# Optimization experiments

Hardware: AMD Instinct MI355X
Metric: run time of the kernel (lower is better)

The kernel has to match this reference:

```python
import jax, jax.numpy as jnp
import numpy as np


def _ln(z, g, b):
    m = z.mean(-1, keepdims=True)
    v = ((z - m) ** 2).mean(-1, keepdims=True)
    return (z - m) * jax.lax.rsqrt(v + 1e-5) * g + b


def _pe(T, D):
    # standard sinusoidal positional encoding (T, D)
    pos = np.arange(T)[:, None]
    i = np.arange(D // 2)[None, :]
    ang = pos / np.power(10000.0, 2.0 * i / D)
    pe = np.zeros((T, D), dtype=np.float32)
    pe[:, 0::2] = np.sin(ang)
    pe[:, 1::2] = np.cos(ang)
    return jnp.asarray(pe)


def _whconv(z, Hinc, filt, W, b):
    # Wavelet hypergraph convolution: psi diag(filt) psi^{-1} Z W + b
    # psi = heat-kernel wavelet of normalized hypergraph Laplacian, 2nd-order Taylor (K=2, s=1)
    S = Hinc.shape[0]
    Dv = Hinc.sum(1) + 1e-6          # node degrees
    De = Hinc.sum(0) + 1e-6          # hyperedge degrees
    Hn = Hinc * (Dv ** -0.5)[:, None]
    A = (Hn / De[None, :]) @ Hn.T    # Dv^-1/2 H De^-1 H^T Dv^-1/2
    I = jnp.eye(S, dtype=z.dtype)
    L = I - A
    L2 = 0.5 * (L @ L)
    psi = I - L + L2                  # exp(-L) approx
    psi_inv = I + L + L2              # exp(+L) approx
    return psi @ (filt[:, None] * (psi_inv @ z)) @ W + b


def setup_inputs():
    S, T, F, D, NS, E, K = 2048, 64, 16, 256, 4, 128, 32
    key = jax.random.key(0)
    ks = iter(jax.random.split(key, 64))
    nrm = lambda shp: jax.random.normal(next(ks), shp, jnp.float32) * 0.02
    return dict(
        x=jax.random.normal(next(ks), (S, T, F), jnp.float32),
        snapshot=(jax.random.uniform(next(ks), (NS, S, E)) < 0.05).astype(jnp.float32),
        params_snapshot=jax.random.uniform(next(ks), (NS,), jnp.float32, 0.0, 0.99),
        beta=jnp.array([0.33, 0.33, 0.33], jnp.float32),
        W_emb=nrm((F, D)), b_emb=jnp.zeros((D,), jnp.float32),
        Wq=nrm((D, D)), bq=jnp.zeros((D,), jnp.float32),
        Wk=nrm((D, D)), bk=jnp.zeros((D,), jnp.float32),
        Wv=nrm((D, D)), bv=jnp.zeros((D,), jnp.float32),
        Wo=nrm((D, D)), bo=jnp.zeros((D,), jnp.float32),
        ln1_g=jnp.ones((D,), jnp.float32), ln1_b=jnp.zeros((D,), jnp.float32),
        W_int=nrm((D, D)), b_int=jnp.zeros((D,), jnp.float32),
        W_mix=nrm((2 * D, D)), b_mix=jnp.zeros((D,), jnp.float32),
        ln2_g=jnp.ones((D,), jnp.float32), ln2_b=jnp.zeros((D,), jnp.float32),
        Wt=nrm((D, D)), bt=jnp.zeros((D,), jnp.float32), vt=nrm((D,)),
        Wh1=nrm((D, D)), bh1=jnp.zeros((D,), jnp.float32), filt1=jnp.ones((S,), jnp.float32),
        Wh2=nrm((D, D)), bh2=jnp.zeros((D,), jnp.float32), filt2=jnp.ones((S,), jnp.float32),
        Wa=nrm((D, D)), Wb=nrm((D, D)), Wg=nrm((D, D)), bg=jnp.zeros((D,), jnp.float32),
        Wm1=nrm((D, D)), bm1=jnp.zeros((D,), jnp.float32),
        Wm2=nrm((D, 1)), bm2=jnp.zeros((1,), jnp.float32),
        num_edges=K,
    )


def reference(x, snapshot, params_snapshot, beta, W_emb, b_emb, Wq, bq, Wk, bk, Wv, bv,
              Wo, bo, ln1_g, ln1_b, W_int, b_int, W_mix, b_mix, ln2_g, ln2_b,
              Wt, bt, vt, Wh1, bh1, filt1, Wh2, bh2, filt2, Wa, Wb, Wg, bg,
              Wm1, bm1, Wm2, bm2, num_edges):
    S, T, _ = x.shape
    D = W_emb.shape[1]
    H = 8
    dh = D // H
    # feature embedding + positional encoding
    h = x @ W_emb + b_emb + _pe(T, D)
    # intra-stock (per-stock temporal) multi-head self-attention + residual + LN
    q = (h @ Wq + bq).reshape(S, T, H, dh)
    k = (h @ Wk + bk).reshape(S, T, H, dh)
    v = (h @ Wv + bv).reshape(S, T, H, dh)
    att = jax.nn.softmax(jnp.einsum('sqhd,skhd->shqk', q, k) / jnp.sqrt(jnp.float32(dh)), axis=-1)
    o = jnp.einsum('shqk,skhd->sqhd', att, v).reshape(S, T, D) @ Wo + bo
    h = _ln(h + o, ln1_g, ln1_b)
    # intensity function + mixing layer (Linear -> ReLU -> LayerNorm)
    intensity = jax.nn.softplus(h @ W_int + b_int)
    z = jax.nn.relu(jnp.concatenate([h, intensity], axis=-1) @ W_mix + b_mix)
    h = _ln(z, ln2_g, ln2_b)
    # temporal attention pooling: (S,T,D) -> (S,D)
    u = jnp.tanh(h @ Wt + bt)
    a = jax.nn.softmax(u @ vt, axis=-1)          # (S,T)
    xs = jnp.einsum('st,std->sd', a, h)           # (S,D)
    # per-snapshot two-layer wavelet hypergraph conv (dropout = eval identity)
    def per_snap(Hinc):
        r1 = jax.nn.leaky_relu(_whconv(xs, Hinc, filt1, Wh1, bh1), 0.1)
        return _whconv(r1, Hinc, filt2, Wh2, bh2)
    reps = jax.vmap(per_snap)(snapshot)           # (NS,S,D)
    hyper = jnp.einsum('n,nsd->sd', params_snapshot, reps)
    # dynamic graph learning: top-k learned similarity graph
    sim = (xs @ Wa) @ (xs @ Wb).T / jnp.sqrt(jnp.float32(D))
    kth = jax.lax.top_k(sim, num_edges)[0][:, -1]
    Adyn = jax.nn.softmax(jnp.where(sim >= kth[:, None], sim, -jnp.inf), axis=-1)
    dyn = jax.nn.relu(Adyn @ xs @ Wg + bg)
    # fusion ('sum' mode) + MLP head
    w = jax.nn.softmax(beta)
    fused = w[0] * xs + w[1] * dyn + w[2] * hyper
    return jax.nn.relu(fused @ Wm1 + bm1) @ Wm2 + bm2   # (S,1)
```

## Files before the change

kernel.cpp:

```cpp
#include <hip/hip_runtime.h>
#include <math.h>

#define S_ 2048
#define T_ 64
#define F_ 16
#define D_ 256
#define NS_ 4
#define E_ 128
#define H_ 8
#define SD_ (S_*D_)
#define PS 264

#define PK_ATT 0
#define PK_WO  393216
#define PK_WI  524288
#define PK_WT  655360
#define PK_WM  786432
#define PKBASE 11674112

typedef __attribute__((ext_vector_type(8))) short bf16x8;
typedef __attribute__((ext_vector_type(4))) float f32x4;

__device__ __forceinline__ float warp_sum64(float v){
  #pragma unroll
  for (int o=32;o>=1;o>>=1) v += __shfl_xor(v,o);
  return v;
}
__device__ __forceinline__ float warp_max64(float v){
  #pragma unroll
  for (int o=32;o>=1;o>>=1) v = fmaxf(v,__shfl_xor(v,o));
  return v;
}
__device__ __forceinline__ float softplus_f(float v){
  return fmaxf(v,0.f) + log1pf(__expf(-fabsf(v)));
}
__device__ __forceinline__ float tanh_f(float v){
  float t = __expf(-2.f*fabsf(v));
  float r = (1.f-t)/(1.f+t);
  return copysignf(r, v);
}
__device__ __forceinline__ void splitf(float f, short& h, short& l){
  unsigned u = __float_as_uint(f);
  unsigned hb = (u + 0x7FFFu + ((u>>16)&1u)) >> 16;
  float fl = f - __uint_as_float(hb<<16);
  unsigned v = __float_as_uint(fl);
  unsigned lb = (v + 0x7FFFu + ((v>>16)&1u)) >> 16;
  h = (short)hb; l = (short)lb;
}
__device__ __forceinline__ f32x4 mfma3(bf16x8 ah, bf16x8 al, bf16x8 bh, bf16x8 bl, f32x4 c){
  c = __builtin_amdgcn_mfma_f32_16x16x32_bf16(al, bh, c, 0,0,0);
  c = __builtin_amdgcn_mfma_f32_16x16x32_bf16(ah, bl, c, 0,0,0);
  c = __builtin_amdgcn_mfma_f32_16x16x32_bf16(ah, bh, c, 0,0,0);
  return c;
}
__device__ __forceinline__ void afrag_f32(const float* base, int stride, int rbase, int ks, int lane, bf16x8& hi, bf16x8& lo){
  const float* p = base + (rbase + (lane&15))*stride + ks + ((lane>>4)<<3);
  #pragma unroll
  for (int jj=0;jj<8;++jj){ short h,l; splitf(p[jj],h,l); hi[jj]=h; lo[jj]=l; }
}
__device__ __forceinline__ bf16x8 afrag_pk(const short* plane, int rbase, int ks, int lane){
  return *(const bf16x8*)(plane + (rbase + (lane&15))*PS + ks + ((lane>>4)<<3));
}
__device__ __forceinline__ void bfrag_pk(const unsigned* pk, int tile, int lane, bf16x8& hi, bf16x8& lo){
  const unsigned* p = pk + (((tile<<6) + lane)<<3);
  #pragma unroll
  for (int jj=0;jj<8;++jj){ unsigned u=p[jj]; hi[jj]=(short)(u & 0xffffu); lo[jj]=(short)(u>>16); }
}
__device__ __forceinline__ void store_h(short* Hh, short* Hl, int r, int c, float f){
  short h,l; splitf(f,h,l);
  Hh[r*PS+c]=h; Hl[r*PS+c]=l;
}
__device__ __forceinline__ float load_h(const short* Hh, const short* Hl, int r, int c){
  int idx=r*PS+c;
  return __uint_as_float(((unsigned)(unsigned short)Hh[idx])<<16)
       + __uint_as_float(((unsigned)(unsigned short)Hl[idx])<<16);
}

__global__ void pack_all(const float* __restrict__ Wq, const float* __restrict__ Wk,
                         const float* __restrict__ Wv, const float* __restrict__ Wo,
                         const float* __restrict__ Wint, const float* __restrict__ Wt,
                         const float* __restrict__ Wmix, short* __restrict__ pkc){
  int y = blockIdx.y;
  int i = blockIdx.x*256 + threadIdx.x;
  if (y < 3){
    const float* W = (y==0)?Wq:((y==1)?Wk:Wv);
    int jj=i&7, n=(i>>3)&15, q=(i>>7)&3, ntg=(i>>9)&15, kt=i>>13;
    float f = W[(kt*32 + q*8 + jj)*256 + (ntg*16+n)];
    short h,l; splitf(f,h,l);
    int hp = ntg>>2, ntl = ntg&3;
    int base = ((hp*8+kt)*6 + y*2)*2048;
    int local = ntl*512 + (q*16+n)*8 + jj;
    short* dst = pkc + PK_ATT;
    dst[base+local] = h;
    dst[base+2048+local] = l;
  } else {
    const float* W; short* dst; int ib = i;
    if (y==3){W=Wo;   dst=pkc+PK_WO;}
    else if (y==4){W=Wint; dst=pkc+PK_WI;}
    else if (y==5){W=Wt;   dst=pkc+PK_WT;}
    else if (y==6){W=Wmix; dst=pkc+PK_WM;}
    else          {W=Wmix; dst=pkc+PK_WM; ib = i + 65536;}
    int jj=ib&7, n=(ib>>3)&15, q=(ib>>7)&3, ntg=(ib>>9)&15, kt=ib>>13;
    float f = W[(kt*32 + q*8 + jj)*256 + (ntg*16+n)];
    short h,l; splitf(f,h,l);
    int dl = kt*16384 + ntg*512 + (q*16+n)*8 + jj;
    dst[dl] = h; dst[dl+8192] = l;
  }
}

__global__ void pe_kernel(float* __restrict__ pe){
  int i = blockIdx.x*256 + threadIdx.x;
  int t = i >> 8, d = i & 255;
  int ii = d >> 1;
  float w = __expf(-(float)ii * (logf(10000.f)/128.f));
  float ang = (float)t * w;
  pe[i] = (d & 1) ? cosf(ang) : sinf(ang);
}

__launch_bounds__(512,1)
__global__ void stageA_kernel(
    const float* __restrict__ x, const float* __restrict__ pe,
    const float* __restrict__ Wemb, const float* __restrict__ bemb,
    const float* __restrict__ bq, const float* __restrict__ bk, const float* __restrict__ bv,
    const float* __restrict__ bo,
    const float* __restrict__ ln1g, const float* __restrict__ ln1b,
    const float* __restrict__ bint,
    const float* __restrict__ bmix,
    const float* __restrict__ ln2g, const float* __restrict__ ln2b,
    const float* __restrict__ bt,
    const float* __restrict__ vt,
    const short* __restrict__ pkc,
    float* __restrict__ xs)
{
  __shared__ __attribute__((aligned(16))) short hbh[64*PS];
  __shared__ __attribute__((aligned(16))) short hbl[64*PS];
  __shared__ __attribute__((aligned(16))) char smem[85504];

  short*    wst   = (short*)smem;
  unsigned* k2f2  = (unsigned*)smem;
  unsigned* v2f2  = (unsigned*)(smem + 16384);
  float*    qb2   = (float*)(smem + 32768);
  float*    scb2  = (float*)(smem + 50176);
  float*    poolb = (float*)smem;

  const int j  = threadIdx.x;
  const int s  = blockIdx.x;
  const int w  = j >> 6;
  const int lane = j & 63;
  const int m_ = lane & 15, qd = lane >> 4;
  const int rg2 = w >> 1, par = w & 1;
  const int rbase = rg2*16;
  const int rv = w*8;
  const int c0 = lane;

  {
    float* xb = (float*)smem;
    const float* xp = x + (long)s*T_*F_;
    for (int i=j; i<T_*F_; i+=512) xb[i] = xp[i];
  }
  __syncthreads();

  {
    const float* xb = (const float*)smem;
    float acc[8][4];
    #pragma unroll
    for (int r=0;r<8;++r){acc[r][0]=0;acc[r][1]=0;acc[r][2]=0;acc[r][3]=0;}
    #pragma unroll
    for (int k=0;k<F_;++k){
      float w0=Wemb[k*D_+c0], w1=Wemb[k*D_+c0+64], w2=Wemb[k*D_+c0+128], w3=Wemb[k*D_+c0+192];
      #pragma unroll
      for (int r=0;r<8;++r){
        float hv = xb[(rv+r)*F_+k];
        acc[r][0]+=hv*w0; acc[r][1]+=hv*w1; acc[r][2]+=hv*w2; acc[r][3]+=hv*w3;
      }
    }
    float b0=bemb[c0],b1=bemb[c0+64],b2=bemb[c0+128],b3=bemb[c0+192];
    __syncthreads();
    #pragma unroll
    for (int r=0;r<8;++r){
      int t = rv+r;
      store_h(hbh,hbl,t,c0,     acc[r][0]+b0+pe[t*D_+c0]);
      store_h(hbh,hbl,t,c0+64,  acc[r][1]+b1+pe[t*D_+c0+64]);
      store_h(hbh,hbl,t,c0+128, acc[r][2]+b2+pe[t*D_+c0+128]);
      store_h(hbh,hbl,t,c0+192, acc[r][3]+b3+pe[t*D_+c0+192]);
    }
  }
  __syncthreads();

  bf16x8 AH[8], AL[8];
  #pragma unroll
  for (int kt=0;kt<8;++kt){
    AH[kt] = afrag_pk(hbh, rbase, kt*32, lane);
    AL[kt] = afrag_pk(hbl, rbase, kt*32, lane);
  }

  const float rs = 0.17677669529663687f;
  f32x4 co[8];
  #pragma unroll
  for (int t=0;t<8;++t) co[t] = (f32x4){0.f,0.f,0.f,0.f};

  for (int hp=0; hp<4; ++hp){
    f32x4 qa[2],ka[2],va[2];
    #pragma unroll
    for (int t=0;t<2;++t){
      qa[t]=(f32x4){0.f,0.f,0.f,0.f};
      ka[t]=(f32x4){0.f,0.f,0.f,0.f};
      va[t]=(f32x4){0.f,0.f,0.f,0.f};
    }
    bf16x8 pre[3];
    {
      const short* b0 = pkc + PK_ATT + (hp*8)*12288;
      #pragma unroll
      for (int r=0;r<3;++r) pre[r] = *(const bf16x8*)(b0 + (j+r*512)*8);
    }
    for (int kt=0; kt<8; ++kt){
      __syncthreads();
      #pragma unroll
      for (int r=0;r<3;++r) *(bf16x8*)(wst + (j+r*512)*8) = pre[r];
      __syncthreads();
      if (kt<7){
        const short* nb = pkc + PK_ATT + (hp*8+kt+1)*12288;
        #pragma unroll
        for (int r=0;r<3;++r) pre[r] = *(const bf16x8*)(nb + (j+r*512)*8);
      }
      bf16x8 ah = AH[kt], al = AL[kt];
      #pragma unroll
      for (int t=0;t<2;++t){
        int ntl = par*2+t;
        bf16x8 bh,bl;
        bh = *(bf16x8*)(wst +         ntl*512 + lane*8);
        bl = *(bf16x8*)(wst + 2048  + ntl*512 + lane*8);
        qa[t]=mfma3(ah,al,bh,bl,qa[t]);
        bh = *(bf16x8*)(wst + 4096  + ntl*512 + lane*8);
        bl = *(bf16x8*)(wst + 6144  + ntl*512 + lane*8);
        ka[t]=mfma3(ah,al,bh,bl,ka[t]);
        bh = *(bf16x8*)(wst + 8192  + ntl*512 + lane*8);
        bl = *(bf16x8*)(wst + 10240 + ntl*512 + lane*8);
        va[t]=mfma3(ah,al,bh,bl,va[t]);
      }
    }
    __syncthreads();
    #pragma unroll
    for (int t=0;t<2;++t){
      int ntg = par*2+t;
      #pragma unroll
      for (int r=0;r<4;++r){
        int trow = rbase + qd*4 + r;
        int pcp = ntg*16 + m_;
        int head = pcp >> 5;
        int cp = pcp & 31;
        int col = hp*64 + pcp;
        qb2[trow*68 + pcp] = (qa[t][r] + bq[col]) * rs;
        short hS,lS;
        float kv2 = ka[t][r] + bk[col];
        splitf(kv2,hS,lS);
        k2f2[head*2048 + (((trow>>4)*4 + (cp>>3))*16 + (trow&15))*8 + (cp&7)]
            = (unsigned)(unsigned short)hS | ((unsigned)(unsigned short)lS<<16);
        float vv2 = va[t][r] + bv[col];
        splitf(vv2,hS,lS);
        v2f2[head*2048 + ((((trow>>5)*2 + (cp>>4))*4 + ((trow>>3)&3))*16 + (cp&15))*8 + (trow&7)]
            = (unsigned)(unsigned short)hS | ((unsigned)(unsigned short)lS<<16);
      }
    }
    __syncthreads();
    float* scb = scb2 + par*4352;
    {
      bf16x8 ah,al;
      afrag_f32(qb2, 68, rbase, par*32, lane, ah, al);
      f32x4 sc4[4];
      #pragma unroll
      for (int nt=0;nt<4;++nt){
        bf16x8 bh,bl; bfrag_pk(k2f2 + par*2048, nt, lane, bh, bl);
        sc4[nt] = mfma3(ah,al,bh,bl,(f32x4){0.f,0.f,0.f,0.f});
      }
      #pragma unroll
      for (int r=0;r<4;++r){
        float mx = fmaxf(fmaxf(sc4[0][r],sc4[1][r]),fmaxf(sc4[2][r],sc4[3][r]));
        #pragma unroll
        for (int o=8;o>=1;o>>=1) mx = fmaxf(mx, __shfl_xor(mx,o));
        float es = 0.f;
        #pragma unroll
        for (int nt=0;nt<4;++nt){ float e=__expf(sc4[nt][r]-mx); sc4[nt][r]=e; es+=e; }
        #pragma unroll
        for (int o=8;o>=1;o>>=1) es += __shfl_xor(es,o);
        float inv = 1.f/es;
        int trow = rbase + qd*4 + r;
        #pragma unroll
        for (int nt=0;nt<4;++nt) scb[trow*68 + nt*16 + m_] = sc4[nt][r]*inv;
      }
    }
    {
      f32x4 oa[2];
      oa[0]=(f32x4){0.f,0.f,0.f,0.f}; oa[1]=(f32x4){0.f,0.f,0.f,0.f};
      #pragma unroll
      for (int kt=0;kt<2;++kt){
        bf16x8 ah2,al2; afrag_f32(scb, 68, rbase, kt*32, lane, ah2, al2);
        #pragma unroll
        for (int nt=0;nt<2;++nt){
          bf16x8 bh,bl; bfrag_pk(v2f2 + par*2048, kt*2+nt, lane, bh, bl);
          oa[nt]=mfma3(ah2,al2,bh,bl,oa[nt]);
        }
      }
      #pragma unroll
      for (int nt=0;nt<2;++nt){
        #pragma unroll
        for (int r=0;r<4;++r)
          qb2[(rbase+qd*4+r)*68 + par*32 + nt*16 + m_] = oa[nt][r];
      }
    }
    __syncthreads();
    for (int ks=0; ks<2; ++ks){
      bf16x8 ah,al; afrag_f32(qb2, 68, rbase, ks*32, lane, ah, al);
      const short* wob = pkc + PK_WO + (hp*2+ks)*16384 + lane*8;
      #pragma unroll
      for (int t=0;t<8;++t){
        int ntg = 2*t+par;
        bf16x8 bh = *(const bf16x8*)(wob + ntg*512);
        bf16x8 bl = *(const bf16x8*)(wob + 8192 + ntg*512);
        co[t]=mfma3(ah,al,bh,bl,co[t]);
      }
    }
  }

  #pragma unroll
  for (int t=0;t<8;++t){
    int cc = (2*t+par)*16+m_;
    float bov = bo[cc];
    #pragma unroll
    for (int r=0;r<4;++r){
      int row = rbase+qd*4+r;
      store_h(hbh,hbl,row,cc, load_h(hbh,hbl,row,cc) + co[t][r] + bov);
    }
  }
  __syncthreads();

  {
    float g0=ln1g[c0],g1=ln1g[c0+64],g2=ln1g[c0+128],g3=ln1g[c0+192];
    float bb0=ln1b[c0],bb1=ln1b[c0+64],bb2=ln1b[c0+128],bb3=ln1b[c0+192];
    for (int rr=0;rr<8;++rr){
      int t=rv+rr;
      float v0=load_h(hbh,hbl,t,c0),    v1=load_h(hbh,hbl,t,c0+64);
      float v2=load_h(hbh,hbl,t,c0+128),v3=load_h(hbh,hbl,t,c0+192);
      float sm=warp_sum64(v0+v1+v2+v3);
      float sq=warp_sum64(v0*v0+v1*v1+v2*v2+v3*v3);
      float mean=sm*(1.f/256.f);
      float inv=rsqrtf(fmaxf(sq*(1.f/256.f)-mean*mean,0.f)+1e-5f);
      store_h(hbh,hbl,t,c0,    (v0-mean)*inv*g0+bb0);
      store_h(hbh,hbl,t,c0+64, (v1-mean)*inv*g1+bb1);
      store_h(hbh,hbl,t,c0+128,(v2-mean)*inv*g2+bb2);
      store_h(hbh,hbl,t,c0+192,(v3-mean)*inv*g3+bb3);
    }
  }
  __syncthreads();

  auto loadB=[&](bf16x8* d, const short* base, int kt){
    const short* p = base + kt*16384 + lane*8;
    d[0]=*(const bf16x8*)(p + (2*w)*512);
    d[1]=*(const bf16x8*)(p + 8192 + (2*w)*512);
    d[2]=*(const bf16x8*)(p + (2*w+1)*512);
    d[3]=*(const bf16x8*)(p + 8192 + (2*w+1)*512);
  };
  const short* BM = pkc + PK_WM;
  const short* BI = pkc + PK_WI;
  const short* BT = pkc + PK_WT;

  f32x4 az[4][2], ai[4][2];
  #pragma unroll
  for (int rt=0;rt<4;++rt){
    az[rt][0]=(f32x4){0.f,0.f,0.f,0.f}; az[rt][1]=(f32x4){0.f,0.f,0.f,0.f};
    ai[rt][0]=(f32x4){0.f,0.f,0.f,0.f}; ai[rt][1]=(f32x4){0.f,0.f,0.f,0.f};
  }
  bf16x8 cb[4], nb[4];
  loadB(cb, BM, 0);
  for (int kt=0; kt<8; ++kt){
    if (kt<7) loadB(nb, BM, kt+1); else loadB(nb, BI, 0);
    #pragma unroll
    for (int rt=0;rt<4;++rt){
      bf16x8 ah = afrag_pk(hbh, rt*16, kt*32, lane);
      bf16x8 al = afrag_pk(hbl, rt*16, kt*32, lane);
      az[rt][0]=mfma3(ah,al,cb[0],cb[1],az[rt][0]);
      az[rt][1]=mfma3(ah,al,cb[2],cb[3],az[rt][1]);
    }
    #pragma unroll
    for (int r=0;r<4;++r) cb[r]=nb[r];
  }
  for (int kt=0; kt<8; ++kt){
    if (kt<7) loadB(nb, BI, kt+1); else loadB(nb, BM, 8);
    #pragma unroll
    for (int rt=0;rt<4;++rt){
      bf16x8 ah = afrag_pk(hbh, rt*16, kt*32, lane);
      bf16x8 al = afrag_pk(hbl, rt*16, kt*32, lane);
      ai[rt][0]=mfma3(ah,al,cb[0],cb[1],ai[rt][0]);
      ai[rt][1]=mfma3(ah,al,cb[2],cb[3],ai[rt][1]);
    }
    #pragma unroll
    for (int r=0;r<4;++r) cb[r]=nb[r];
  }
  __syncthreads();
  #pragma unroll
  for (int rt=0;rt<4;++rt){
    #pragma unroll
    for (int t=0;t<2;++t){
      int col=(2*w+t)*16+m_;
      float bb=bint[col];
      #pragma unroll
      for (int r=0;r<4;++r)
        store_h(hbh,hbl, rt*16+qd*4+r, col, softplus_f(ai[rt][t][r]+bb));
    }
  }
  __syncthreads();
  for (int kt=0; kt<8; ++kt){
    if (kt<7) loadB(nb, BM, kt+9); else loadB(nb, BT, 0);
    #pragma unroll
    for (int rt=0;rt<4;++rt){
      bf16x8 ah = afrag_pk(hbh, rt*16, kt*32, lane);
      bf16x8 al = afrag_pk(hbl, rt*16, kt*32, lane);
      az[rt][0]=mfma3(ah,al,cb[0],cb[1],az[rt][0]);
      az[rt][1]=mfma3(ah,al,cb[2],cb[3],az[rt][1]);
    }
    #pragma unroll
    for (int r=0;r<4;++r) cb[r]=nb[r];
  }
  __syncthreads();
  #pragma unroll
  for (int rt=0;rt<4;++rt){
    #pragma unroll
    for (int t=0;t<2;++t){
      int col=(2*w+t)*16+m_;
      float bb=bmix[col];
      #pragma unroll
      for (int r=0;r<4;++r)
        store_h(hbh,hbl, rt*16+qd*4+r, col, fmaxf(az[rt][t][r]+bb,0.f));
    }
  }
  __syncthreads();
  {
    float g0=ln2g[c0],g1=ln2g[c0+64],g2=ln2g[c0+128],g3=ln2g[c0+192];
    float bb0=ln2b[c0],bb1=ln2b[c0+64],bb2=ln2b[c0+128],bb3=ln2b[c0+192];
    for (int rr=0;rr<8;++rr){
      int t=rv+rr;
      float v0=load_h(hbh,hbl,t,c0),    v1=load_h(hbh,hbl,t,c0+64);
      float v2=load_h(hbh,hbl,t,c0+128),v3=load_h(hbh,hbl,t,c0+192);
      float sm=warp_sum64(v0+v1+v2+v3);
      float sq=warp_sum64(v0*v0+v1*v1+v2*v2+v3*v3);
      float mean=sm*(1.f/256.f);
      float inv=rsqrtf(fmaxf(sq*(1.f/256.f)-mean*mean,0.f)+1e-5f);
      store_h(hbh,hbl,t,c0,    (v0-mean)*inv*g0+bb0);
      store_h(hbh,hbl,t,c0+64, (v1-mean)*inv*g1+bb1);
      store_h(hbh,hbl,t,c0+128,(v2-mean)*inv*g2+bb2);
      store_h(hbh,hbl,t,c0+192,(v3-mean)*inv*g3+bb3);
    }
  }
  __syncthreads();
  {
    f32x4 at4[4][2];
    #pragma unroll
    for (int rt=0;rt<4;++rt){
      at4[rt][0]=(f32x4){0.f,0.f,0.f,0.f}; at4[rt][1]=(f32x4){0.f,0.f,0.f,0.f};
    }
    for (int kt=0; kt<8; ++kt){
      if (kt<7) loadB(nb, BT, kt+1);
      #pragma unroll
      for (int rt=0;rt<4;++rt){
        bf16x8 ah = afrag_pk(hbh, rt*16, kt*32, lane);
        bf16x8 al = afrag_pk(hbl, rt*16, kt*32, lane);
        at4[rt][0]=mfma3(ah,al,cb[0],cb[1],at4[rt][0]);
        at4[rt][1]=mfma3(ah,al,cb[2],cb[3],at4[rt][1]);
      }
      #pragma unroll
      for (int r=0;r<4;++r) cb[r]=nb[r];
    }
    #pragma unroll
    for (int rt=0;rt<4;++rt){
      #pragma unroll
      for (int r=0;r<4;++r){
        int row = rt*16+qd*4+r;
        float p = 0.f;
        #pragma unroll
        for (int t=0;t<2;++t){
          int col=(2*w+t)*16+m_;
          p += tanh_f(at4[rt][t][r]+bt[col])*vt[col];
        }
        p += __shfl_xor(p,1); p += __shfl_xor(p,2);
        p += __shfl_xor(p,4); p += __shfl_xor(p,8);
        if (m_==0) poolb[w*64+row] = p;
      }
    }
  }
  __syncthreads();
  if (j < 64){
    float v = 0.f;
    #pragma unroll
    for (int ww=0;ww<8;++ww) v += poolb[ww*64+j];
    float m = warp_max64(v);
    float e = __expf(v-m);
    float ssum = warp_sum64(e);
    poolb[512+j] = e/ssum;
  }
  __syncthreads();
  if (j < 256){
    float acc=0.f;
    #pragma unroll 8
    for (int t=0;t<T_;++t) acc += poolb[512+t]*load_h(hbh,hbl,t,j);
    xs[(long)s*D_+j] = acc;
  }
}

__global__ void hg_deg(const float* __restrict__ Hinc, float* __restrict__ Dv, float* __restrict__ De){
  const int n = blockIdx.y, s0 = blockIdx.x*64;
  const float* Hp = Hinc + (long)n*S_*E_;
  const int j = threadIdx.x;
  {
    int r = j>>2, q = j&3;
    const float* rp = Hp + (long)(s0+r)*E_ + q*32;
    float sm=0;
    #pragma unroll
    for (int e=0;e<32;++e) sm += rp[e];
    sm += __shfl_xor(sm,1); sm += __shfl_xor(sm,2);
    if (q==0) Dv[n*S_+s0+r]=sm+1e-6f;
  }
  if (j < E_){
    float cs=0;
    for (int ss=0;ss<64;++ss) cs += Hp[(long)(s0+ss)*E_+j];
    atomicAdd(&De[n*E_+j], cs);
  }
}

__global__ void build_ecsr(const float* __restrict__ snap, const float* __restrict__ Dv,
                           int* __restrict__ ei, float* __restrict__ ev, int* __restrict__ ecnt){
  __shared__ int cnts[257];
  const int e = blockIdx.x, n = blockIdx.y, t = threadIdx.x;
  const float* col = snap + (long)n*S_*E_ + e;
  int loc[8]; int c=0;
  #pragma unroll
  for (int r=0;r<8;++r){
    int s = t*8+r;
    if (col[(long)s*E_] != 0.f) loc[c++]=s;
  }
  cnts[t+1]=c;
  __syncthreads();
  if (t==0){ cnts[0]=0; for (int i=1;i<=256;++i) cnts[i]+=cnts[i-1]; }
  __syncthreads();
  int base = cnts[t];
  long eb = ((long)n*E_+e)*256;
  for (int k=0;k<c;++k){
    int pos = base+k;
    if (pos<256){ ei[eb+pos]=loc[k]; ev[eb+pos]=rsqrtf(Dv[n*S_+loc[k]]); }
  }
  if (t==255) ecnt[n*E_+e] = min(cnts[256],256);
}
__global__ void build_scsr(const float* __restrict__ snap, const float* __restrict__ Dv,
                           const float* __restrict__ De,
                           int* __restrict__ si, float* __restrict__ sv, int* __restrict__ scnt){
  const int s = blockIdx.x*256+threadIdx.x, n = blockIdx.y;
  const float* row = snap + ((long)n*S_+s)*E_;
  float vs = rsqrtf(Dv[n*S_+s]);
  long sb = ((long)n*S_+s)*32;
  int c=0;
  for (int e=0;e<E_;++e){
    if (row[e]!=0.f && c<32){
      si[sb+c]=e;
      sv[sb+c]=vs/(De[n*E_+e]+1e-6f);
      ++c;
    }
  }
  scnt[n*S_+s]=c;
}

__launch_bounds__(256,4)
__global__ void hg_p1(const int* __restrict__ ei, const float* __restrict__ ev,
                      const int* __restrict__ ecnt,
                      const float* __restrict__ M, long mz, float* __restrict__ P){
  __shared__ int sidx[256];
  __shared__ float sval[256];
  const int e = blockIdx.x, n = blockIdx.y, d = threadIdx.x;
  long eb = ((long)n*E_+e)*256;
  const int c = ecnt[n*E_+e];
  if (d < c){ sidx[d]=ei[eb+d]; sval[d]=ev[eb+d]; }
  __syncthreads();
  const float* Mp = M + (long)n*mz;
  float a0=0.f,a1=0.f,a2=0.f,a3=0.f;
  int i=0;
  for (; i+4<=c; i+=4){
    float m0 = Mp[(long)sidx[i+0]*D_+d];
    float m1 = Mp[(long)sidx[i+1]*D_+d];
    float m2 = Mp[(long)sidx[i+2]*D_+d];
    float m3 = Mp[(long)sidx[i+3]*D_+d];
    a0 += sval[i+0]*m0; a1 += sval[i+1]*m1;
    a2 += sval[i+2]*m2; a3 += sval[i+3]*m3;
  }
  for (; i<c; ++i) a0 += sval[i]*Mp[(long)sidx[i]*D_+d];
  P[((long)n*E_+e)*D_+d] = (a0+a1)+(a2+a3);
}
__launch_bounds__(256,4)
__global__ void hg_p2(const int* __restrict__ si, const float* __restrict__ sv,
                      const int* __restrict__ scnt, const float* __restrict__ P,
                      const float* __restrict__ X1, long x1z, float c1,
                      const float* __restrict__ X2, long x2z, float c2,
                      float c3, const float* __restrict__ filt, int usefilt,
                      float* __restrict__ out){
  __shared__ int sidx[8][32];
  __shared__ float sval[8][32];
  __shared__ int scc[8];
  const int s0 = blockIdx.x*8, n = blockIdx.y, d = threadIdx.x;
  {
    int k = d>>5, i = d&31;
    long sb = ((long)n*S_+s0+k)*32;
    sidx[k][i] = si[sb+i];
    sval[k][i] = sv[sb+i];
    if (i==0) scc[k] = scnt[n*S_+s0+k];
  }
  __syncthreads();
  const float* Pn = P + (long)n*E_*D_;
  #pragma unroll
  for (int k=0;k<8;++k){
    int s = s0+k;
    int c = scc[k];
    float acc=0.f;
    for (int i=0;i<c;++i) acc += sval[k][i]*Pn[(long)sidx[k][i]*D_+d];
    long li=(long)s*D_+d;
    float v=c3*acc;
    if (X1) v+=c1*X1[x1z*n+li];
    if (X2) v+=c2*X2[x2z*n+li];
    out[((long)n*S_+s)*D_+d]=(usefilt?filt[s]:1.f)*v;
  }
}

__launch_bounds__(256,1)
__global__ void gemm_nn(const float* __restrict__ A, long az,
                        const float* __restrict__ B, long bz,
                        float* __restrict__ C, long cz,
                        int K, int N,
                        const float* __restrict__ bias, int act)
{
  __shared__ float al[32*68];
  __shared__ float bl[32*68];
  const int mt = blockIdx.x*64, nt = blockIdx.y*64, zz = blockIdx.z;
  const int j = threadIdx.x;
  const float* Ap = A + (long)az*zz;
  const float* Bp = B + (long)bz*zz;
  const int tx = j&15, ty = j>>4;
  float acc[4][4];
  #pragma unroll
  for (int i=0;i<4;++i){acc[i][0]=0;acc[i][1]=0;acc[i][2]=0;acc[i][3]=0;}
  for (int k0=0;k0<K;k0+=32){
    #pragma unroll
    for (int half=0; half<2; ++half){
      int idx = j + half*256;
      int r = idx>>3, kk=(idx&7)*4;
      float4 v = *(const float4*)&Ap[(long)(mt+r)*K + k0+kk];
      al[(kk+0)*68+r]=v.x; al[(kk+1)*68+r]=v.y; al[(kk+2)*68+r]=v.z; al[(kk+3)*68+r]=v.w;
    }
    #pragma unroll
    for (int half=0; half<2; ++half){
      int idx = j + half*256;
      int r = idx>>4, cc=(idx&15)*4;
      *(float4*)&bl[r*68+cc] = *(const float4*)&Bp[(long)(k0+r)*N + nt+cc];
    }
    __syncthreads();
    #pragma unroll
    for (int kk=0;kk<32;++kk){
      float4 a = *(const float4*)&al[kk*68+ty*4];
      float4 b = *(const float4*)&bl[kk*68+tx*4];
      acc[0][0]+=a.x*b.x; acc[0][1]+=a.x*b.y; acc[0][2]+=a.x*b.z; acc[0][3]+=a.x*b.w;
      acc[1][0]+=a.y*b.x; acc[1][1]+=a.y*b.y; acc[1][2]+=a.y*b.z; acc[1][3]+=a.y*b.w;
      acc[2][0]+=a.z*b.x; acc[2][1]+=a.z*b.y; acc[2][2]+=a.z*b.z; acc[2][3]+=a.z*b.w;
      acc[3][0]+=a.w*b.x; acc[3][1]+=a.w*b.y; acc[3][2]+=a.w*b.z; acc[3][3]+=a.w*b.w;
    }
    __syncthreads();
  }
  #pragma unroll
  for (int i=0;i<4;++i){
    int row = mt+ty*4+i;
    #pragma unroll
    for (int m=0;m<4;++m){
      int col = nt+tx*4+m;
      float v = acc[i][m];
      if (bias) v += bias[col];
      if (act==1) v = fmaxf(v,0.f);
      else if (act==2) v = (v>0.f)? v : 0.1f*v;
      C[(long)cz*zz + (long)row*N + col] = v;
    }
  }
}

__launch_bounds__(256,1)
__global__ void gemm_nt_scaled(const float* __restrict__ A, const float* __restrict__ B,
                               float* __restrict__ C, int K, float scale)
{
  __shared__ float al[32*68];
  __shared__ float bl[32*68];
  const int mt = blockIdx.x*64, nt = blockIdx.y*64;
  const int j = threadIdx.x;
  const int tx = j&15, ty = j>>4;
  float acc[4][4];
  #pragma unroll
  for (int i=0;i<4;++i){acc[i][0]=0;acc[i][1]=0;acc[i][2]=0;acc[i][3]=0;}
  for (int k0=0;k0<K;k0+=32){
    #pragma unroll
    for (int half=0; half<2; ++half){
      int idx = j + half*256;
      int r = idx>>3, kk=(idx&7)*4;
      float4 v = *(const float4*)&A[(long)(mt+r)*K + k0+kk];
      al[(kk+0)*68+r]=v.x; al[(kk+1)*68+r]=v.y; al[(kk+2)*68+r]=v.z; al[(kk+3)*68+r]=v.w;
    }
    #pragma unroll
    for (int half=0; half<2; ++half){
      int idx = j + half*256;
      int r = idx>>3, kk=(idx&7)*4;
      float4 v = *(const float4*)&B[(long)(nt+r)*K + k0+kk];
      bl[(kk+0)*68+r]=v.x; bl[(kk+1)*68+r]=v.y; bl[(kk+2)*68+r]=v.z; bl[(kk+3)*68+r]=v.w;
    }
    __syncthreads();
    #pragma unroll
    for (int kk=0;kk<32;++kk){
      float4 a = *(const float4*)&al[kk*68+ty*4];
      float4 b = *(const float4*)&bl[kk*68+tx*4];
      acc[0][0]+=a.x*b.x; acc[0][1]+=a.x*b.y; acc[0][2]+=a.x*b.z; acc[0][3]+=a.x*b.w;
      acc[1][0]+=a.y*b.x; acc[1][1]+=a.y*b.y; acc[1][2]+=a.y*b.z; acc[1][3]+=a.y*b.w;
      acc[2][0]+=a.z*b.x; acc[2][1]+=a.z*b.y; acc[2][2]+=a.z*b.z; acc[2][3]+=a.z*b.w;
      acc[3][0]+=a.w*b.x; acc[3][1]+=a.w*b.y; acc[3][2]+=a.w*b.z; acc[3][3]+=a.w*b.w;
    }
    __syncthreads();
  }
  #pragma unroll
  for (int i=0;i<4;++i){
    #pragma unroll
    for (int m=0;m<4;++m){
      C[(long)(mt+ty*4+i)*S_ + nt+tx*4+m] = acc[i][m]*scale;
    }
  }
}

__launch_bounds__(256,4)
__global__ void topk_gather(const float* __restrict__ sim, const float* __restrict__ xs,
                            const int* __restrict__ Kp, float* __restrict__ dynpre)
{
  __shared__ float wred[4]; __shared__ int ired[4];
  __shared__ float selw[256]; __shared__ int seli[256];
  __shared__ int cnt; __shared__ float sh_kth, sh_max, sh_den; __shared__ int sh_bi;
  const int s = blockIdx.x, j = threadIdx.x;
  const float* rp = sim + (long)s*S_;
  float vo[8], v[8];
  *(float4*)&vo[0] = *(const float4*)&rp[j*8];
  *(float4*)&vo[4] = *(const float4*)&rp[j*8+4];
  #pragma unroll
  for (int r=0;r<8;++r) v[r]=vo[r];
  if (j==0) cnt=0;
  const int K = Kp[0];
  for (int it=0; it<K; ++it){
    float m=-3.0e38f; int mi=0;
    #pragma unroll
    for (int r=0;r<8;++r){ if (v[r]>m){m=v[r]; mi=r;} }
    mi += j*8;
    #pragma unroll
    for (int o=32;o>=1;o>>=1){
      float om=__shfl_xor(m,o); int oi=__shfl_xor(mi,o);
      if (om>m){m=om;mi=oi;}
    }
    if ((j&63)==0){ wred[j>>6]=m; ired[j>>6]=mi; }
    __syncthreads();
    if (j==0){
      float bm=wred[0]; int bi=ired[0];
      #pragma unroll
      for (int w=1;w<4;++w) if (wred[w]>bm){bm=wred[w];bi=ired[w];}
      sh_kth=bm; sh_bi=bi;
      if (it==0) sh_max=bm;
    }
    __syncthreads();
    int sel = sh_bi - j*8;
    #pragma unroll
    for (int r=0;r<8;++r) if (r==sel) v[r] = -3.0e38f;
  }
  const float kth=sh_kth, rmax=sh_max;
  #pragma unroll
  for (int r=0;r<8;++r){
    if (vo[r]>=kth){
      int p=atomicAdd(&cnt,1);
      if (p<256){ seli[p]=j*8+r; selw[p]=__expf(vo[r]-rmax); }
    }
  }
  __syncthreads();
  int c = cnt; if (c>256) c=256;
  {
    float p = (j<c)? selw[j] : 0.f;
    p = warp_sum64(p);
    if ((j&63)==0) wred[j>>6]=p;
    __syncthreads();
    if (j==0) sh_den = wred[0]+wred[1]+wred[2]+wred[3];
    __syncthreads();
  }
  float acc=0.f;
  for (int l=0;l<c;++l) acc += selw[l]*xs[(long)seli[l]*D_ + j];
  dynpre[(long)s*D_+j] = acc / sh_den;
}

__global__ void hyperwsum_kernel(const float* __restrict__ reps, const float* __restrict__ ps,
                                 float* __restrict__ hyper)
{
  long idx = (long)blockIdx.x*256+threadIdx.x;
  hyper[idx] = ps[0]*reps[idx] + ps[1]*reps[(long)SD_+idx]
             + ps[2]*reps[2L*SD_+idx] + ps[3]*reps[3L*SD_+idx];
}

__global__ void fuse_kernel(const float* __restrict__ xs, const float* __restrict__ dyn,
                            const float* __restrict__ hyper, const float* __restrict__ beta,
                            float* __restrict__ fused)
{
  long idx = (long)blockIdx.x*256+threadIdx.x;
  float b0=beta[0],b1=beta[1],b2=beta[2];
  float mx=fmaxf(b0,fmaxf(b1,b2));
  float e0=__expf(b0-mx),e1=__expf(b1-mx),e2=__expf(b2-mx);
  float inv=1.f/(e0+e1+e2);
  fused[idx] = e0*inv*xs[idx] + e1*inv*dyn[idx] + e2*inv*hyper[idx];
}

__global__ void head_kernel(const float* __restrict__ hh1, const float* __restrict__ Wm2,
                            const float* __restrict__ bm2, float* __restrict__ out)
{
  int r = blockIdx.x*32 + (threadIdx.x>>3);
  int sub = threadIdx.x&7;
  const float* hp = hh1 + (long)r*D_;
  float acc=0.f;
  for (int c=sub;c<D_;c+=8) acc += hp[c]*Wm2[c];
  acc += __shfl_xor(acc,1); acc += __shfl_xor(acc,2); acc += __shfl_xor(acc,4);
  if (sub==0) out[r]=acc+bm2[0];
}

extern "C" void kernel_launch(void* const* d_in, const int* in_sizes, int n_in,
                              void* d_out, int out_size, void* d_ws, size_t ws_size,
                              hipStream_t stream)
{
  (void)in_sizes;(void)n_in;(void)out_size;(void)ws_size;
  const float* x        =(const float*)d_in[0];
  const float* snapshot =(const float*)d_in[1];
  const float* ps       =(const float*)d_in[2];
  const float* beta     =(const float*)d_in[3];
  const float* Wemb=(const float*)d_in[4];  const float* bemb=(const float*)d_in[5];
  const float* Wq  =(const float*)d_in[6];  const float* bq  =(const float*)d_in[7];
  const float* Wk  =(const float*)d_in[8];  const float* bk  =(const float*)d_in[9];
  const float* Wv  =(const float*)d_in[10]; const float* bv  =(const float*)d_in[11];
  const float* Wo  =(const float*)d_in[12]; const float* bo  =(const float*)d_in[13];
  const float* ln1g=(const float*)d_in[14]; const float* ln1b=(const float*)d_in[15];
  const float* Wint=(const float*)d_in[16]; const float* bint=(const float*)d_in[17];
  const float* Wmix=(const float*)d_in[18]; const float* bmix=(const float*)d_in[19];
  const float* ln2g=(const float*)d_in[20]; const float* ln2b=(const float*)d_in[21];
  const float* Wt  =(const float*)d_in[22]; const float* bt  =(const float*)d_in[23];
  const float* vt  =(const float*)d_in[24];
  const float* Wh1 =(const float*)d_in[25]; const float* bh1 =(const float*)d_in[26];
  const float* filt1=(const float*)d_in[27];
  const float* Wh2 =(const float*)d_in[28]; const float* bh2 =(const float*)d_in[29];
  const float* filt2=(const float*)d_in[30];
  const float* Wa  =(const float*)d_in[31]; const float* Wb  =(const float*)d_in[32];
  const float* Wg  =(const float*)d_in[33]; const float* bg  =(const float*)d_in[34];
  const float* Wm1 =(const float*)d_in[35]; const float* bm1 =(const float*)d_in[36];
  const float* Wm2 =(const float*)d_in[37]; const float* bm2 =(const float*)d_in[38];
  const int* numedges=(const int*)d_in[39];
  float* out=(float*)d_out;

  float* w = (float*)d_ws;
  float* pe    = w;
  float* repsb = w;
  float* sim   = w;
  float* P     = w + 4194304;
  float* Dv    = P + 131072;
  float* De    = Dv + 8192;
  int*   ecnt  = (int*)(De + 512);
  int*   scnt  = ecnt + 512;
  int*   ei    = scnt + 8192;
  float* ev    = (float*)(ei + 131072);
  int*   si    = (int*)(ev + 131072);
  float* sv    = (float*)(si + 262144);
  float* xs    = w + 6431232;
  float* hyper = xs + SD_;
  float* bufA  = hyper + SD_;
  float* bufB  = bufA + 4*SD_;
  float* p1    = bufA;
  float* q1    = bufA + SD_;
  float* dynpre= bufA + 2*SD_;
  float* dyn   = bufA + 3*SD_;
  float* fused = bufB;
  float* hh1   = bufB + SD_;
  short* pkc   = (short*)(w + PKBASE);

  hipMemsetAsync(De, 0, (size_t)NS_*E_*sizeof(float), stream);
  pe_kernel<<<64,256,0,stream>>>(pe);
  pack_all<<<dim3(256,8),256,0,stream>>>(Wq,Wk,Wv,Wo,Wint,Wt,Wmix,pkc);

  stageA_kernel<<<S_,512,0,stream>>>(x,pe,Wemb,bemb,bq,bk,bv,bo,
                                     ln1g,ln1b,bint,bmix,ln2g,ln2b,bt,vt,
                                     pkc,xs);
  hg_deg<<<dim3(32,NS_),256,0,stream>>>(snapshot,Dv,De);
  build_ecsr<<<dim3(E_,NS_),256,0,stream>>>(snapshot,Dv,ei,ev,ecnt);
  build_scsr<<<dim3(8,NS_),256,0,stream>>>(snapshot,Dv,De,si,sv,scnt);

  auto applyA=[&](const float* M, long mz,
                  const float* X1, long x1z, float c1,
                  const float* X2, long x2z, float c2, float c3,
                  const float* filt, int uf, float* outb){
    hg_p1<<<dim3(E_,NS_),256,0,stream>>>(ei,ev,ecnt,M,mz,P);
    hg_p2<<<dim3(S_/8,NS_),256,0,stream>>>(si,sv,scnt,P,X1,x1z,c1,X2,x2z,c2,c3,filt,uf,outb);
  };

  applyA(xs,0,     xs,0,1.f,    nullptr,0,0.f,  -1.f,  nullptr,0, bufA);
  applyA(bufA,SD_, xs,0,1.f,    bufA,SD_,1.5f,  -0.5f, filt1,1,   bufB);
  applyA(bufB,SD_, bufB,SD_,1.f, nullptr,0,0.f, -1.f,  nullptr,0, bufA);
  applyA(bufA,SD_, bufB,SD_,1.f, bufA,SD_,-0.5f,-0.5f, nullptr,0, bufA);
  gemm_nn<<<dim3(32,4,NS_),256,0,stream>>>(bufA,SD_, Wh1,0, bufB,SD_, 256,256, bh1, 2);

  applyA(bufB,SD_, bufB,SD_,1.f, nullptr,0,0.f, -1.f,  nullptr,0, bufA);
  applyA(bufA,SD_, bufB,SD_,1.f, bufA,SD_,1.5f, -0.5f, filt2,1,   bufB);
  applyA(bufB,SD_, bufB,SD_,1.f, nullptr,0,0.f, -1.f,  nullptr,0, bufA);
  applyA(bufA,SD_, bufB,SD_,1.f, bufA,SD_,-0.5f,-0.5f, nullptr,0, bufA);
  gemm_nn<<<dim3(32,4,NS_),256,0,stream>>>(bufA,SD_, Wh2,0, repsb,SD_, 256,256, bh2, 0);
  hyperwsum_kernel<<<2048,256,0,stream>>>(repsb,ps,hyper);

  gemm_nn<<<dim3(32,4,1),256,0,stream>>>(xs,0, Wa,0, p1,0, 256,256, nullptr, 0);
  gemm_nn<<<dim3(32,4,1),256,0,stream>>>(xs,0, Wb,0, q1,0, 256,256, nullptr, 0);
  gemm_nt_scaled<<<dim3(32,32),256,0,stream>>>(p1,q1,sim,256,0.0625f);
  topk_gather<<<S_,256,0,stream>>>(sim,xs,numedges,dynpre);
  gemm_nn<<<dim3(32,4,1),256,0,stream>>>(dynpre,0, Wg,0, dyn,0, 256,256, bg, 1);

  fuse_kernel<<<2048,256,0,stream>>>(xs,dyn,hyper,beta,fused);
  gemm_nn<<<dim3(32,4,1),256,0,stream>>>(fused,0, Wm1,0, hh1,0, 256,256, bm1, 1);
  head_kernel<<<64,256,0,stream>>>(hh1,Wm2,bm2,out);
}
```

Baseline: 1.449 ms.

## Replace FP32 SIMT GEMMs with split-bf16 MFMA GEMMs using prepacked weights

The remaining scalar FP32 tiled GEMMs (hypergraph projections, dynamic-graph projections, similarity, Wg and Wm1) are replaced by MFMA kernels that split fp32 into hi/lo bf16 pairs, a three-product emulation that keeps near-fp32 accuracy. Six more weight matrices are packed into MFMA fragment layout inside the existing pack kernel, so B operands load directly as vectors. The NT similarity GEMM splits both operands on the fly. The A operand is read straight from global memory without LDS staging, which may cost memory efficiency, and the packed weights occupy a new workspace region.

After: 1.548 ms. 1.07x slower.

```diff
diff --git a/kernel.cpp b/kernel.cpp
--- a/kernel.cpp
+++ b/kernel.cpp
@@ -17,6 +17,13 @@
 #define PK_WT  655360
 #define PK_WM  786432
 #define PKBASE 11674112
+#define PK2BASE 5242880
+#define PKH1 0
+#define PKH2 131072
+#define PKA  262144
+#define PKB  393216
+#define PKG  524288
+#define PKM1 655360
 
 typedef __attribute__((ext_vector_type(8))) short bf16x8;
 typedef __attribute__((ext_vector_type(4))) float f32x4;
@@ -79,7 +86,11 @@
 __global__ void pack_all(const float* __restrict__ Wq, const float* __restrict__ Wk,
                          const float* __restrict__ Wv, const float* __restrict__ Wo,
                          const float* __restrict__ Wint, const float* __restrict__ Wt,
-                         const float* __restrict__ Wmix, short* __restrict__ pkc){
+                         const float* __restrict__ Wmix,
+                         const float* __restrict__ Wh1, const float* __restrict__ Wh2,
+                         const float* __restrict__ Wa, const float* __restrict__ Wb,
+                         const float* __restrict__ Wg, const float* __restrict__ Wm1,
+                         short* __restrict__ pkc, short* __restrict__ pk2){
   int y = blockIdx.y;
   int i = blockIdx.x*256 + threadIdx.x;
   if (y < 3){
@@ -99,7 +110,13 @@
     else if (y==4){W=Wint; dst=pkc+PK_WI;}
     else if (y==5){W=Wt;   dst=pkc+PK_WT;}
     else if (y==6){W=Wmix; dst=pkc+PK_WM;}
-    else          {W=Wmix; dst=pkc+PK_WM; ib = i + 65536;}
+    else if (y==7){W=Wmix; dst=pkc+PK_WM; ib = i + 65536;}
+    else if (y==8){W=Wh1;  dst=pk2+PKH1;}
+    else if (y==9){W=Wh2;  dst=pk2+PKH2;}
+    else if (y==10){W=Wa;  dst=pk2+PKA;}
+    else if (y==11){W=Wb;  dst=pk2+PKB;}
+    else if (y==12){W=Wg;  dst=pk2+PKG;}
+    else          {W=Wm1;  dst=pk2+PKM1;}
     int jj=ib&7, n=(ib>>3)&15, q=(ib>>7)&3, ntg=(ib>>9)&15, kt=ib>>13;
     float f = W[(kt*32 + q*8 + jj)*256 + (ntg*16+n)];
     short h,l; splitf(f,h,l);
@@ -626,109 +643,81 @@
   }
 }
 
-__launch_bounds__(256,1)
-__global__ void gemm_nn(const float* __restrict__ A, long az,
-                        const float* __restrict__ B, long bz,
-                        float* __restrict__ C, long cz,
-                        int K, int N,
-                        const float* __restrict__ bias, int act)
+__launch_bounds__(256,4)
+__global__ void gemm_pk(const float* __restrict__ A, const short* __restrict__ Bpk,
+                        float* __restrict__ C, const float* __restrict__ bias, int act)
 {
-  __shared__ float al[32*68];
-  __shared__ float bl[32*68];
-  const int mt = blockIdx.x*64, nt = blockIdx.y*64, zz = blockIdx.z;
   const int j = threadIdx.x;
-  const float* Ap = A + (long)az*zz;
-  const float* Bp = B + (long)bz*zz;
-  const int tx = j&15, ty = j>>4;
-  float acc[4][4];
-  #pragma unroll
-  for (int i=0;i<4;++i){acc[i][0]=0;acc[i][1]=0;acc[i][2]=0;acc[i][3]=0;}
-  for (int k0=0;k0<K;k0+=32){
-    #pragma unroll
-    for (int half=0; half<2; ++half){
-      int idx = j + half*256;
-      int r = idx>>3, kk=(idx&7)*4;
-      float4 v = *(const float4*)&Ap[(long)(mt+r)*K + k0+kk];
-      al[(kk+0)*68+r]=v.x; al[(kk+1)*68+r]=v.y; al[(kk+2)*68+r]=v.z; al[(kk+3)*68+r]=v.w;
-    }
-    #pragma unroll
-    for (int half=0; half<2; ++half){
-      int idx = j + half*256;
-      int r = idx>>4, cc=(idx&15)*4;
-      *(float4*)&bl[r*68+cc] = *(const float4*)&Bp[(long)(k0+r)*N + nt+cc];
-    }
-    __syncthreads();
-    #pragma unroll
-    for (int kk=0;kk<32;++kk){
-      float4 a = *(const float4*)&al[kk*68+ty*4];
-      float4 b = *(const float4*)&bl[kk*68+tx*4];
-      acc[0][0]+=a.x*b.x; acc[0][1]+=a.x*b.y; acc[0][2]+=a.x*b.z; acc[0][3]+=a.x*b.w;
-      acc[1][0]+=a.y*b.x; acc[1][1]+=a.y*b.y; acc[1][2]+=a.y*b.z; acc[1][3]+=a.y*b.w;
-      acc[2][0]+=a.z*b.x; acc[2][1]+=a.z*b.y; acc[2][2]+=a.z*b.z; acc[2][3]+=a.z*b.w;
-      acc[3][0]+=a.w*b.x; acc[3][1]+=a.w*b.y; acc[3][2]+=a.w*b.z; acc[3][3]+=a.w*b.w;
-    }
-    __syncthreads();
-  }
-  #pragma unroll
-  for (int i=0;i<4;++i){
-    int row = mt+ty*4+i;
-    #pragma unroll
-    for (int m=0;m<4;++m){
-      int col = nt+tx*4+m;
-      float v = acc[i][m];
-      if (bias) v += bias[col];
-      if (act==1) v = fmaxf(v,0.f);
-      else if (act==2) v = (v>0.f)? v : 0.1f*v;
-      C[(long)cz*zz + (long)row*N + col] = v;
-    }
-  }
-}
-
-__launch_bounds__(256,1)
-__global__ void gemm_nt_scaled(const float* __restrict__ A, const float* __restrict__ B,
-                               float* __restrict__ C, int K, float scale)
+  const int w = j>>6, lane = j&63;
+  const int m_ = lane&15, qd = lane>>4;
+  const long r0 = (long)blockIdx.x*64 + w*16;
+  f32x4 acc[16];
+  #pragma unroll
+  for (int nt=0;nt<16;++nt) acc[nt]=(f32x4){0.f,0.f,0.f,0.f};
+  #pragma unroll
+  for (int kt=0; kt<8; ++kt){
+    bf16x8 ah, al;
+    {
+      const float* p = A + (r0 + m_)*D_ + kt*32 + (qd<<3);
+      #pragma unroll
+      for (int jj=0;jj<8;++jj){ short h,l; splitf(p[jj],h,l); ah[jj]=h; al[jj]=l; }
+    }
+    const short* bp = Bpk + kt*16384 + lane*8;
+    #pragma unroll
+    for (int nt=0;nt<16;++nt){
+      bf16x8 bh = *(const bf16x8*)(bp + nt*512);
+      bf16x8 bl = *(const bf16x8*)(bp + 8192 + nt*512);
+      acc[nt]=mfma3(ah,al,bh,bl,acc[nt]);
+    }
+  }
+  #pragma unroll
+  for (int nt=0;nt<16;++nt){
+    int col = nt*16+m_;
+    float bb = bias ? bias[col] : 0.f;
+    #pragma unroll
+    for (int r=0;r<4;++r){
+      float v = acc[nt][r]+bb;
+      if (act==1) v=fmaxf(v,0.f);
+      else if (act==2) v=(v>0.f)?v:0.1f*v;
+      C[(r0+qd*4+r)*D_ + col] = v;
+    }
+  }
+}
+
+__launch_bounds__(256,4)
+__global__ void gemm_nt_pk(const float* __restrict__ A, const float* __restrict__ B,
+                           float* __restrict__ C, float scale)
 {
-  __shared__ float al[32*68];
-  __shared__ float bl[32*68];
-  const int mt = blockIdx.x*64, nt = blockIdx.y*64;
   const int j = threadIdx.x;
-  const int tx = j&15, ty = j>>4;
-  float acc[4][4];
-  #pragma unroll
-  for (int i=0;i<4;++i){acc[i][0]=0;acc[i][1]=0;acc[i][2]=0;acc[i][3]=0;}
-  for (int k0=0;k0<K;k0+=32){
-    #pragma unroll
-    for (int half=0; half<2; ++half){
-      int idx = j + half*256;
-      int r = idx>>3, kk=(idx&7)*4;
-      float4 v = *(const float4*)&A[(long)(mt+r)*K + k0+kk];
-      al[(kk+0)*68+r]=v.x; al[(kk+1)*68+r]=v.y; al[(kk+2)*68+r]=v.z; al[(kk+3)*68+r]=v.w;
-    }
-    #pragma unroll
-    for (int half=0; half<2; ++half){
-      int idx = j + half*256;
-      int r = idx>>3, kk=(idx&7)*4;
-      float4 v = *(const float4*)&B[(long)(nt+r)*K + k0+kk];
-      bl[(kk+0)*68+r]=v.x; bl[(kk+1)*68+r]=v.y; bl[(kk+2)*68+r]=v.z; bl[(kk+3)*68+r]=v.w;
-    }
-    __syncthreads();
-    #pragma unroll
-    for (int kk=0;kk<32;++kk){
-      float4 a = *(const float4*)&al[kk*68+ty*4];
-      float4 b = *(const float4*)&bl[kk*68+tx*4];
-      acc[0][0]+=a.x*b.x; acc[0][1]+=a.x*b.y; acc[0][2]+=a.x*b.z; acc[0][3]+=a.x*b.w;
-      acc[1][0]+=a.y*b.x; acc[1][1]+=a.y*b.y; acc[1][2]+=a.y*b.z; acc[1][3]+=a.y*b.w;
-      acc[2][0]+=a.z*b.x; acc[2][1]+=a.z*b.y; acc[2][2]+=a.z*b.z; acc[2][3]+=a.z*b.w;
-      acc[3][0]+=a.w*b.x; acc[3][1]+=a.w*b.y; acc[3][2]+=a.w*b.z; acc[3][3]+=a.w*b.w;
-    }
-    __syncthreads();
-  }
-  #pragma unroll
-  for (int i=0;i<4;++i){
-    #pragma unroll
-    for (int m=0;m<4;++m){
-      C[(long)(mt+ty*4+i)*S_ + nt+tx*4+m] = acc[i][m]*scale;
-    }
+  const int w = j>>6, lane = j&63;
+  const int m_ = lane&15, qd = lane>>4;
+  const long r0 = (long)blockIdx.x*64 + w*16;
+  const long c0 = (long)blockIdx.y*64;
+  f32x4 acc[4];
+  #pragma unroll
+  for (int nt=0;nt<4;++nt) acc[nt]=(f32x4){0.f,0.f,0.f,0.f};
+  #pragma unroll
+  for (int kt=0; kt<8; ++kt){
+    bf16x8 ah, al;
+    {
+      const float* p = A + (r0 + m_)*D_ + kt*32 + (qd<<3);
+      #pragma unroll
+      for (int jj=0;jj<8;++jj){ short h,l; splitf(p[jj],h,l); ah[jj]=h; al[jj]=l; }
+    }
+    #pragma unroll
+    for (int nt=0;nt<4;++nt){
+      bf16x8 bh, bl;
+      const float* p = B + (c0 + nt*16 + m_)*D_ + kt*32 + (qd<<3);
+      #pragma unroll
+      for (int jj=0;jj<8;++jj){ short h,l; splitf(p[jj],h,l); bh[jj]=h; bl[jj]=l; }
+      acc[nt]=mfma3(ah,al,bh,bl,acc[nt]);
+    }
+  }
+  #pragma unroll
+  for (int nt=0;nt<4;++nt){
+    #pragma unroll
+    for (int r=0;r<4;++r)
+      C[(r0+qd*4+r)*S_ + c0 + nt*16 + m_] = acc[nt][r]*scale;
   }
 }
 
@@ -871,6 +860,7 @@
   float* ev    = (float*)(ei + 131072);
   int*   si    = (int*)(ev + 131072);
   float* sv    = (float*)(si + 262144);
+  short* pk2   = (short*)(w + PK2BASE);
   float* xs    = w + 6431232;
   float* hyper = xs + SD_;
   float* bufA  = hyper + SD_;
@@ -885,7 +875,8 @@
 
   hipMemsetAsync(De, 0, (size_t)NS_*E_*sizeof(float), stream);
   pe_kernel<<<64,256,0,stream>>>(pe);
-  pack_all<<<dim3(256,8),256,0,stream>>>(Wq,Wk,Wv,Wo,Wint,Wt,Wmix,pkc);
+  pack_all<<<dim3(256,14),256,0,stream>>>(Wq,Wk,Wv,Wo,Wint,Wt,Wmix,
+                                          Wh1,Wh2,Wa,Wb,Wg,Wm1,pkc,pk2);
 
   stageA_kernel<<<S_,512,0,stream>>>(x,pe,Wemb,bemb,bq,bk,bv,bo,
                                      ln1g,ln1b,bint,bmix,ln2g,ln2b,bt,vt,
@@ -906,22 +897,22 @@
   applyA(bufA,SD_, xs,0,1.f,    bufA,SD_,1.5f,  -0.5f, filt1,1,   bufB);
   applyA(bufB,SD_, bufB,SD_,1.f, nullptr,0,0.f, -1.f,  nullptr,0, bufA);
   applyA(bufA,SD_, bufB,SD_,1.f, bufA,SD_,-0.5f,-0.5f, nullptr,0, bufA);
-  gemm_nn<<<dim3(32,4,NS_),256,0,stream>>>(bufA,SD_, Wh1,0, bufB,SD_, 256,256, bh1, 2);
+  gemm_pk<<<128,256,0,stream>>>(bufA, pk2+PKH1, bufB, bh1, 2);
 
   applyA(bufB,SD_, bufB,SD_,1.f, nullptr,0,0.f, -1.f,  nullptr,0, bufA);
   applyA(bufA,SD_, bufB,SD_,1.f, bufA,SD_,1.5f, -0.5f, filt2,1,   bufB);
   applyA(bufB,SD_, bufB,SD_,1.f, nullptr,0,0.f, -1.f,  nullptr,0, bufA);
   applyA(bufA,SD_, bufB,SD_,1.f, bufA,SD_,-0.5f,-0.5f, nullptr,0, bufA);
-  gemm_nn<<<dim3(32,4,NS_),256,0,stream>>>(bufA,SD_, Wh2,0, repsb,SD_, 256,256, bh2, 0);
+  gemm_pk<<<128,256,0,stream>>>(bufA, pk2+PKH2, repsb, bh2, 0);
   hyperwsum_kernel<<<2048,256,0,stream>>>(repsb,ps,hyper);
 
-  gemm_nn<<<dim3(32,4,1),256,0,stream>>>(xs,0, Wa,0, p1,0, 256,256, nullptr, 0);
-  gemm_nn<<<dim3(32,4,1),256,0,stream>>>(xs,0, Wb,0, q1,0, 256,256, nullptr, 0);
-  gemm_nt_scaled<<<dim3(32,32),256,0,stream>>>(p1,q1,sim,256,0.0625f);
+  gemm_pk<<<32,256,0,stream>>>(xs, pk2+PKA, p1, nullptr, 0);
+  gemm_pk<<<32,256,0,stream>>>(xs, pk2+PKB, q1, nullptr, 0);
+  gemm_nt_pk<<<dim3(32,32),256,0,stream>>>(p1,q1,sim,0.0625f);
   topk_gather<<<S_,256,0,stream>>>(sim,xs,numedges,dynpre);
-  gemm_nn<<<dim3(32,4,1),256,0,stream>>>(dynpre,0, Wg,0, dyn,0, 256,256, bg, 1);
+  gemm_pk<<<32,256,0,stream>>>(dynpre, pk2+PKG, dyn, bg, 1);
 
   fuse_kernel<<<2048,256,0,stream>>>(xs,dyn,hyper,beta,fused);
-  gemm_nn<<<dim3(32,4,1),256,0,stream>>>(fused,0, Wm1,0, hh1,0, 256,256, bm1, 1);
+  gemm_pk<<<32,256,0,stream>>>(fused, pk2+PKM1, hh1, bm1, 1);
   head_kernel<<<64,256,0,stream>>>(hh1,Wm2,bm2,out);
 }
```
